# Kernel optimization log

Measured on AMD Instinct MI355X. Metric: run time of the kernel, lower is better.

Reference implementation:

```python
import jax, jax.numpy as jnp
import numpy as np

B, C, H, W = 8, 512, 32, 32
NUM_HEADS = 8
HEAD_DIM = C // NUM_HEADS


def setup_inputs() -> dict:
    key = jax.random.key(0)
    k1, k2, k3 = jax.random.split(key, 3)
    s = 0.02
    return {
        "x": jax.random.normal(k1, (B, C, H, W), dtype=jnp.float32),
        "W_qkv": jax.random.normal(k2, (3 * C, C), dtype=jnp.float32) * s,
        "b_qkv": jnp.zeros((3 * C,), dtype=jnp.float32),
        "W_proj": jax.random.normal(k3, (C, C), dtype=jnp.float32) * s,
        "b_proj": jnp.zeros((C,), dtype=jnp.float32),
    }


def reference(x, W_qkv, b_qkv, W_proj, b_proj):
    b, c, h, w = x.shape
    n = h * w  # seq_len in raster order
    nh, hd = NUM_HEADS, c // NUM_HEADS
    scale = hd ** -0.5

    # b c h w -> b n c
    x_seq = x.reshape(b, c, n).transpose(0, 2, 1)
    qkv = x_seq @ W_qkv.T + b_qkv  # (b, n, 3c)
    # b n (3 nh hd) -> 3, b, nh, n, hd
    qkv = qkv.reshape(b, n, 3, nh, hd).transpose(2, 0, 3, 1, 4)
    q, k, v = qkv[0], qkv[1], qkv[2]

    attn = jnp.einsum('bhnd,bhmd->bhnm', q, k) * scale
    causal = jnp.tril(jnp.ones((n, n), dtype=bool))
    attn = jnp.where(causal, attn, -jnp.inf)
    attn = jax.nn.softmax(attn, axis=-1)

    out = jnp.einsum('bhnm,bhmd->bhnd', attn, v)
    out = out.transpose(0, 2, 1, 3).reshape(b, n, c)  # b n c
    out = out @ W_proj.T + b_proj
    # b (h w) c -> b c h w
    return out.transpose(0, 2, 1).reshape(b, c, h, w)
```

## Files before the change

### kernel.cpp

```cpp
#include <hip/hip_runtime.h>
#include <hip/hip_bf16.h>
#include <math.h>

#define B_  8
#define C_  512
#define N_  1024
#define NH_ 8
#define HD_ 64
#define C3_ 1536

typedef __bf16 bf16x8 __attribute__((ext_vector_type(8)));
typedef float  f32x4  __attribute__((ext_vector_type(4)));
typedef __hip_bfloat16 bf16;

__device__ __forceinline__ f32x4 mfma16(const bf16x8& a, const bf16x8& b, const f32x4& c) {
    return __builtin_amdgcn_mfma_f32_16x16x32_bf16(a, b, c, 0, 0, 0);
}

__device__ __forceinline__ void ld_lds16(const bf16* g, bf16* l_uniform) {
    __builtin_amdgcn_global_load_lds(
        (const __attribute__((address_space(1))) void*)(uintptr_t)g,
        (__attribute__((address_space(3))) void*)(uintptr_t)l_uniform,
        16, 0, 0);
}


__global__ __launch_bounds__(256) void cvt_w(const float* __restrict__ Wq,
                                             const float* __restrict__ Wp,
                                             bf16* __restrict__ Wqb,
                                             bf16* __restrict__ Wpb) {
    int i = blockIdx.x * 256 + threadIdx.x;
    if (i < C3_ * C_) Wqb[i] = __float2bfloat16(Wq[i]);
    else {
        int j = i - C3_ * C_;
        if (j < C_ * C_) Wpb[j] = __float2bfloat16(Wp[j]);
    }
}

__global__ __launch_bounds__(256) void transpose_x(const float* __restrict__ x,
                                                   bf16* __restrict__ xb) {
    __shared__ float T[32][33];
    const int n0 = blockIdx.x * 32, c0 = blockIdx.y * 32, b = blockIdx.z;
    const int tx = threadIdx.x, ty = threadIdx.y;
    const float* xp = x + ((size_t)b * C_ + c0) * N_ + n0;
#pragma unroll
    for (int l = 0; l < 4; ++l)
        T[ty + 8 * l][tx] = xp[(ty + 8 * l) * N_ + tx];
    __syncthreads();
    bf16* xo = xb + ((size_t)b * N_ + n0) * C_ + c0;
#pragma unroll
    for (int l = 0; l < 4; ++l)
        xo[(ty + 8 * l) * C_ + tx] = __float2bfloat16(T[tx][ty + 8 * l]);
}

__global__ __launch_bounds__(256) void qkv_mfma(const bf16* __restrict__ xb,
                                                const bf16* __restrict__ Wqb,
                                                const float* __restrict__ bq,
                                                bf16* __restrict__ Qb,
                                                bf16* __restrict__ Kb,
                                                bf16* __restrict__ Vt) {
    __shared__ bf16 As[128 * 32];
    __shared__ bf16 Bs[128 * 32];
    __shared__ bf16 Vl[4][16][20];
    const int tid = threadIdx.x, w = tid >> 6, lane = tid & 63;
    const int lo = lane & 15, hi = lane >> 4;
    const int j0 = blockIdx.x * 128;
    const int m0 = blockIdx.y * 128;
    const int b  = m0 >> 10;

    const int srow = w * 32 + (lane >> 2);
    const int scol = (lane & 3) * 8;
    const bf16* gA = xb  + (size_t)(m0 + srow) * C_ + scol;
    const bf16* gB = Wqb + (size_t)(j0 + srow) * C_ + scol;
    bf16* lA = As + (w * 32) * 32;
    bf16* lB = Bs + (w * 32) * 32;

    f32x4 acc[4][4];
#pragma unroll
    for (int mt = 0; mt < 4; ++mt)
#pragma unroll
        for (int jt = 0; jt < 4; ++jt)
            acc[mt][jt] = (f32x4){0.f, 0.f, 0.f, 0.f};

    for (int k0 = 0; k0 < C_; k0 += 32) {
        ld_lds16(gA + k0, lA);
        ld_lds16(gA + (size_t)16 * C_ + k0, lA + 16 * 32);
        ld_lds16(gB + k0, lB);
        ld_lds16(gB + (size_t)16 * C_ + k0, lB + 16 * 32);
        __syncthreads();

        bf16x8 af[4], bfr[4];
#pragma unroll
        for (int mt = 0; mt < 4; ++mt)
            af[mt] = *(const bf16x8*)(As + ((w & 1) * 64 + mt * 16 + lo) * 32 + hi * 8);
#pragma unroll
        for (int jt = 0; jt < 4; ++jt)
            bfr[jt] = *(const bf16x8*)(Bs + ((w >> 1) * 64 + jt * 16 + lo) * 32 + hi * 8);
#pragma unroll
        for (int mt = 0; mt < 4; ++mt)
#pragma unroll
            for (int jt = 0; jt < 4; ++jt)
                acc[mt][jt] = mfma16(af[mt], bfr[jt], acc[mt][jt]);
        __syncthreads();
    }

    const int jb = (w >> 1) * 64;
    const int nbase = (m0 & 1023) + (w & 1) * 64;
#pragma unroll
    for (int jt = 0; jt < 4; ++jt) {
        const int j16 = j0 + jb + jt * 16;
        const float bias = bq[j16 + lo];
        if (j16 < 512) {
            const int h = j16 >> 6, d = (j16 & 63) + lo;
            bf16* qp = Qb + ((size_t)(b * NH_ + h) * N_) * HD_ + d;
#pragma unroll
            for (int mt = 0; mt < 4; ++mt)
#pragma unroll
                for (int r = 0; r < 4; ++r) {
                    int n = nbase + mt * 16 + hi * 4 + r;
                    qp[(size_t)n * HD_] = __float2bfloat16((acc[mt][jt][r] + bias) * 0.125f);
                }
        } else if (j16 < 1024) {
            const int jj = j16 - 512;
            const int h = jj >> 6, d = (jj & 63) + lo;
            bf16* kp = Kb + ((size_t)(b * NH_ + h) * N_) * HD_ + d;
#pragma unroll
            for (int mt = 0; mt < 4; ++mt)
#pragma unroll
                for (int r = 0; r < 4; ++r) {
                    int n = nbase + mt * 16 + hi * 4 + r;
                    kp[(size_t)n * HD_] = __float2bfloat16(acc[mt][jt][r] + bias);
                }
        } else {
            const int jj = j16 - 1024;
            const int h = jj >> 6, dbase = jj & 63;
            bf16* vp = Vt + ((size_t)(b * NH_ + h) * HD_ + dbase) * N_ + nbase;
#pragma unroll
            for (int mt = 0; mt < 4; ++mt) {
#pragma unroll
                for (int r = 0; r < 4; ++r)
                    Vl[w][hi * 4 + r][lo] = __float2bfloat16(acc[mt][jt][r] + bias);
#pragma unroll
                for (int r = 0; r < 4; ++r)
                    vp[(size_t)(hi * 4 + r) * N_ + mt * 16 + lo] = Vl[w][lo][hi * 4 + r];
            }
        }
    }
}


__global__ __launch_bounds__(256) void attn_mfma(const bf16* __restrict__ Qb,
                                                 const bf16* __restrict__ Kb,
                                                 const bf16* __restrict__ Vt,
                                                 bf16* __restrict__ ao) {
    __shared__ bf16 Ks0[64 * 32], Ks1[64 * 32];
    __shared__ bf16 Vs0[64 * 32], Vs1[64 * 32];
    __shared__ __align__(16) bf16 Pl[4][2][2][16][40];

    const int tid  = threadIdx.x;
    const int wv   = tid >> 6;
    const int lane = tid & 63;
    const int lo   = lane & 15;
    const int hi   = lane >> 4;
    const int bh   = blockIdx.x & 63;
    const int blk  = blockIdx.x >> 6;
    const int pi   = blk * 4 + wv;
    const int qwA  = pi * 16;
    const int qwB  = (63 - pi) * 16;

    const bf16* Qh = Qb + (size_t)bh * N_ * HD_;
    const bf16* Kh = Kb + (size_t)bh * N_ * HD_;
    const bf16* Vh = Vt + (size_t)bh * HD_ * N_;

    const bf16x8 qA0 = *(const bf16x8*)(Qh + (qwA + lo) * HD_ + hi * 8);
    const bf16x8 qA1 = *(const bf16x8*)(Qh + (qwA + lo) * HD_ + 32 + hi * 8);
    const bf16x8 qB0 = *(const bf16x8*)(Qh + (qwB + lo) * HD_ + hi * 8);
    const bf16x8 qB1 = *(const bf16x8*)(Qh + (qwB + lo) * HD_ + 32 + hi * 8);

    const int srow = tid >> 2;
    const int scol = (tid & 3) * 8;
    const bf16* gK = Kh + (size_t)srow * HD_ + scol;
    const bf16* gV = Vh + (size_t)srow * N_ + scol;
    bf16* lK0 = Ks0 + wv * 512;
    bf16* lK1 = Ks1 + wv * 512;
    bf16* lV0 = Vs0 + wv * 512;
    bf16* lV1 = Vs1 + wv * 512;

    f32x4 OA[4], OB[4];
    float LA[4], LB[4];
#pragma unroll
    for (int r = 0; r < 4; ++r) {
        OA[0][r] = OA[1][r] = OA[2][r] = OA[3][r] = 0.f;
        OB[0][r] = OB[1][r] = OB[2][r] = OB[3][r] = 0.f;
        LA[r] = 0.f; LB[r] = 0.f;
    }

    const int nkbA   = (qwA + 79) >> 6;
    const int nkbB   = (qwB + 79) >> 6;
    const int nkbBlk = ((63 - blk * 4) * 16 + 79) >> 6;

    for (int kb = 0; kb < nkbBlk; ++kb) {
        const int key0 = kb * 64;

        ld_lds16(gK + (size_t)key0 * HD_,      lK0);
        ld_lds16(gK + (size_t)key0 * HD_ + 32, lK1);
        ld_lds16(gV + key0,                    lV0);
        ld_lds16(gV + key0 + 32,               lV1);
        __syncthreads();

        if (kb < nkbB) {
            const bool doA = (kb < nkbA);

            bf16x8 kf[4][2], vf[4][2];
#pragma unroll
            for (int t = 0; t < 4; ++t) {
                kf[t][0] = *(const bf16x8*)(Ks0 + (t * 16 + lo) * 32 + hi * 8);
                kf[t][1] = *(const bf16x8*)(Ks1 + (t * 16 + lo) * 32 + hi * 8);
                vf[t][0] = *(const bf16x8*)(Vs0 + (t * 16 + lo) * 32 + hi * 8);
                vf[t][1] = *(const bf16x8*)(Vs1 + (t * 16 + lo) * 32 + hi * 8);
            }

            f32x4 SB[4], SA[4];
#pragma unroll
            for (int t = 0; t < 4; ++t) {
                SB[t] = (f32x4){0.f, 0.f, 0.f, 0.f};
                SB[t] = mfma16(qB0, kf[t][0], SB[t]);
                SB[t] = mfma16(qB1, kf[t][1], SB[t]);
            }
            if (doA) {
#pragma unroll
                for (int t = 0; t < 4; ++t) {
                    SA[t] = (f32x4){0.f, 0.f, 0.f, 0.f};
                    SA[t] = mfma16(qA0, kf[t][0], SA[t]);
                    SA[t] = mfma16(qA1, kf[t][1], SA[t]);
                }
            }

            if (key0 + 63 > qwB) {
#pragma unroll
                for (int t = 0; t < 4; ++t)
#pragma unroll
                    for (int r = 0; r < 4; ++r)
                        if (key0 + t * 16 + lo > qwB + hi * 4 + r) SB[t][r] = -1e30f;
            }
            if (doA && key0 + 63 > qwA) {
#pragma unroll
                for (int t = 0; t < 4; ++t)
#pragma unroll
                    for (int r = 0; r < 4; ++r)
                        if (key0 + t * 16 + lo > qwA + hi * 4 + r) SA[t][r] = -1e30f;
            }

#pragma unroll
            for (int t = 0; t < 4; ++t)
#pragma unroll
                for (int r = 0; r < 4; ++r) {
                    float p = __expf(SB[t][r]);
                    LB[r] += p;
                    Pl[wv][1][t >> 1][hi * 4 + r][(t & 1) * 16 + lo] = __float2bfloat16(p);
                }
            if (doA) {
#pragma unroll
                for (int t = 0; t < 4; ++t)
#pragma unroll
                    for (int r = 0; r < 4; ++r) {
                        float p = __expf(SA[t][r]);
                        LA[r] += p;
                        Pl[wv][0][t >> 1][hi * 4 + r][(t & 1) * 16 + lo] = __float2bfloat16(p);
                    }
            }

            bf16x8 paB0 = *(const bf16x8*)(&Pl[wv][1][0][lo][hi * 8]);
            bf16x8 paB1 = *(const bf16x8*)(&Pl[wv][1][1][lo][hi * 8]);
#pragma unroll
            for (int t = 0; t < 4; ++t) {
                OB[t] = mfma16(paB0, vf[t][0], OB[t]);
                OB[t] = mfma16(paB1, vf[t][1], OB[t]);
            }
            if (doA) {
                bf16x8 paA0 = *(const bf16x8*)(&Pl[wv][0][0][lo][hi * 8]);
                bf16x8 paA1 = *(const bf16x8*)(&Pl[wv][0][1][lo][hi * 8]);
#pragma unroll
                for (int t = 0; t < 4; ++t) {
                    OA[t] = mfma16(paA0, vf[t][0], OA[t]);
                    OA[t] = mfma16(paA1, vf[t][1], OA[t]);
                }
            }
        }
        __syncthreads();
    }

    const int b = bh >> 3, h = bh & 7;
#pragma unroll
    for (int c = 0; c < 2; ++c) {
        const int qw = c ? qwB : qwA;
        f32x4* O = c ? OB : OA;
        float* Lp = c ? LB : LA;
        float rL[4];
#pragma unroll
        for (int r = 0; r < 4; ++r) {
            float Ls = Lp[r];
#pragma unroll
            for (int off = 1; off < 16; off <<= 1)
                Ls += __shfl_xor(Ls, off, 64);
            rL[r] = 1.f / Ls;
        }
#pragma unroll
        for (int t = 0; t < 4; ++t)
#pragma unroll
            for (int r = 0; r < 4; ++r) {
                int q = qw + hi * 4 + r;
                ao[((size_t)b * N_ + q) * C_ + h * HD_ + t * 16 + lo] =
                    __float2bfloat16(O[t][r] * rL[r]);
            }
    }
}

__global__ __launch_bounds__(256) void proj_mfma(const bf16* __restrict__ aob,
                                                 const bf16* __restrict__ Wpb,
                                                 const float* __restrict__ bp,
                                                 float* __restrict__ out) {
    __shared__ bf16 As[64 * 32];
    __shared__ bf16 Bs[128 * 32];
    const int tid = threadIdx.x, w = tid >> 6, lane = tid & 63;
    const int lo = lane & 15, hi = lane >> 4;
    const int j0 = blockIdx.x * 64;
    const int n0 = blockIdx.y * 128;
    const int b  = n0 >> 10;

    const int r4 = lane >> 2, c8 = (lane & 3) * 8;
    const bf16* gA = Wpb + (size_t)(j0 + w * 16 + r4) * C_ + c8;
    const bf16* gB = aob + (size_t)(n0 + w * 32 + r4) * C_ + c8;
    bf16* lA = As + (w * 16) * 32;
    bf16* lB = Bs + (w * 32) * 32;

    f32x4 acc[2][4];
#pragma unroll
    for (int mt = 0; mt < 2; ++mt)
#pragma unroll
        for (int jt = 0; jt < 4; ++jt)
            acc[mt][jt] = (f32x4){0.f, 0.f, 0.f, 0.f};

    for (int k0 = 0; k0 < C_; k0 += 32) {
        ld_lds16(gA + k0, lA);
        ld_lds16(gB + k0, lB);
        ld_lds16(gB + (size_t)16 * C_ + k0, lB + 16 * 32);
        __syncthreads();

        bf16x8 af[2], bfr[4];
#pragma unroll
        for (int mt = 0; mt < 2; ++mt)
            af[mt] = *(const bf16x8*)(As + ((w & 1) * 32 + mt * 16 + lo) * 32 + hi * 8);
#pragma unroll
        for (int jt = 0; jt < 4; ++jt)
            bfr[jt] = *(const bf16x8*)(Bs + ((w >> 1) * 64 + jt * 16 + lo) * 32 + hi * 8);
#pragma unroll
        for (int mt = 0; mt < 2; ++mt)
#pragma unroll
            for (int jt = 0; jt < 4; ++jt)
                acc[mt][jt] = mfma16(af[mt], bfr[jt], acc[mt][jt]);
        __syncthreads();
    }

#pragma unroll
    for (int mt = 0; mt < 2; ++mt)
#pragma unroll
        for (int r = 0; r < 4; ++r) {
            const int j = j0 + (w & 1) * 32 + mt * 16 + hi * 4 + r;
            const float bias = bp[j];
            float* op = out + ((size_t)(b * C_ + j)) * N_ + (n0 & 1023) + (w >> 1) * 64 + lo;
#pragma unroll
            for (int jt = 0; jt < 4; ++jt)
                op[jt * 16] = acc[mt][jt][r] + bias;
        }
}

extern "C" void kernel_launch(void* const* d_in, const int* in_sizes, int n_in,
                              void* d_out, int out_size, void* d_ws, size_t ws_size,
                              hipStream_t stream) {
    const float* x  = (const float*)d_in[0];
    const float* Wq = (const float*)d_in[1];
    const float* bq = (const float*)d_in[2];
    const float* Wp = (const float*)d_in[3];
    const float* bp = (const float*)d_in[4];
    float* out = (float*)d_out;

    const size_t headElems = (size_t)B_ * NH_ * N_ * HD_;
    bf16* xb  = (bf16*)d_ws;
    bf16* Wqb = xb + (size_t)B_ * N_ * C_;
    bf16* Wpb = Wqb + (size_t)C3_ * C_;
    bf16* Qb  = Wpb + (size_t)C_ * C_;
    bf16* Kb  = Qb + headElems;
    bf16* Vt  = Kb + headElems;
    bf16* aob = Vt + headElems;

    cvt_w<<<dim3((C3_ * C_ + C_ * C_ + 255) / 256), dim3(256), 0, stream>>>(Wq, Wp, Wqb, Wpb);
    transpose_x<<<dim3(N_ / 32, C_ / 32, B_), dim3(32, 8), 0, stream>>>(x, xb);

    qkv_mfma<<<dim3(C3_ / 128, (B_ * N_) / 128), dim3(256), 0, stream>>>(xb, Wqb, bq, Qb, Kb, Vt);
    attn_mfma<<<dim3(8 * 64), dim3(256), 0, stream>>>(Qb, Kb, Vt, aob);
    proj_mfma<<<dim3(C_ / 64, (B_ * N_) / 128), dim3(256), 0, stream>>>(aob, Wpb, bp, out);
}
```

Measured before the change: 142.4 us.

## Double-buffer attention K/V tiles and fuse input prep kernels

```diff
diff --git a/kernel.cpp b/kernel.cpp
--- a/kernel.cpp
+++ b/kernel.cpp
@@ -9,8 +9,9 @@
 #define HD_ 64
 #define C3_ 1536
 
-typedef __bf16 bf16x8 __attribute__((ext_vector_type(8)));
-typedef float  f32x4  __attribute__((ext_vector_type(4)));
+typedef __bf16 bf16x8  __attribute__((ext_vector_type(8)));
+typedef __bf16 bf16x4v __attribute__((ext_vector_type(4)));
+typedef float  f32x4   __attribute__((ext_vector_type(4)));
 typedef __hip_bfloat16 bf16;
 
 __device__ __forceinline__ f32x4 mfma16(const bf16x8& a, const bf16x8& b, const f32x4& c) {
@@ -24,33 +25,42 @@
         16, 0, 0);
 }
 
-
-__global__ __launch_bounds__(256) void cvt_w(const float* __restrict__ Wq,
-                                             const float* __restrict__ Wp,
-                                             bf16* __restrict__ Wqb,
-                                             bf16* __restrict__ Wpb) {
-    int i = blockIdx.x * 256 + threadIdx.x;
-    if (i < C3_ * C_) Wqb[i] = __float2bfloat16(Wq[i]);
-    else {
-        int j = i - C3_ * C_;
-        if (j < C_ * C_) Wpb[j] = __float2bfloat16(Wp[j]);
-    }
-}
-
-__global__ __launch_bounds__(256) void transpose_x(const float* __restrict__ x,
-                                                   bf16* __restrict__ xb) {
-    __shared__ float T[32][33];
-    const int n0 = blockIdx.x * 32, c0 = blockIdx.y * 32, b = blockIdx.z;
-    const int tx = threadIdx.x, ty = threadIdx.y;
-    const float* xp = x + ((size_t)b * C_ + c0) * N_ + n0;
-#pragma unroll
-    for (int l = 0; l < 4; ++l)
-        T[ty + 8 * l][tx] = xp[(ty + 8 * l) * N_ + tx];
-    __syncthreads();
-    bf16* xo = xb + ((size_t)b * N_ + n0) * C_ + c0;
-#pragma unroll
-    for (int l = 0; l < 4; ++l)
-        xo[(ty + 8 * l) * C_ + tx] = __float2bfloat16(T[tx][ty + 8 * l]);
+__global__ __launch_bounds__(256) void prep(const float* __restrict__ x,
+                                            const float* __restrict__ Wq,
+                                            const float* __restrict__ Wp,
+                                            bf16* __restrict__ xb,
+                                            bf16* __restrict__ Wqb,
+                                            bf16* __restrict__ Wpb) {
+    const int tid = threadIdx.x;
+    if (blockIdx.x < 4096) {
+        __shared__ float T[32][33];
+        int t = blockIdx.x;
+        const int n0 = (t & 31) * 32; t >>= 5;
+        const int c0 = (t & 15) * 32; t >>= 4;
+        const int b  = t;
+        const int tx = tid & 31, ty = tid >> 5;
+        const float* xp = x + ((size_t)b * C_ + c0) * N_ + n0;
+#pragma unroll
+        for (int l = 0; l < 4; ++l)
+            T[ty + 8 * l][tx] = xp[(ty + 8 * l) * N_ + tx];
+        __syncthreads();
+        bf16* xo = xb + ((size_t)b * N_ + n0) * C_ + c0;
+#pragma unroll
+        for (int l = 0; l < 4; ++l)
+            xo[(ty + 8 * l) * C_ + tx] = __float2bfloat16(T[tx][ty + 8 * l]);
+    } else {
+        const int base = (blockIdx.x - 4096) * 1024 + tid * 4;
+        const float* src;
+        bf16* dst;
+        int off;
+        if (base < C3_ * C_) { src = Wq; dst = Wqb; off = base; }
+        else                 { src = Wp; dst = Wpb; off = base - C3_ * C_; }
+        f32x4 w = *(const f32x4*)(src + off);
+        bf16x4v o;
+#pragma unroll
+        for (int i = 0; i < 4; ++i) o[i] = (__bf16)w[i];
+        *(bf16x4v*)(dst + off) = o;
+    }
 }
 
 __global__ __launch_bounds__(256) void qkv_mfma(const bf16* __restrict__ xb,
@@ -153,8 +163,8 @@
                                                  const bf16* __restrict__ Kb,
                                                  const bf16* __restrict__ Vt,
                                                  bf16* __restrict__ ao) {
-    __shared__ bf16 Ks0[64 * 32], Ks1[64 * 32];
-    __shared__ bf16 Vs0[64 * 32], Vs1[64 * 32];
+    __shared__ bf16 Ks0[2][64 * 32], Ks1[2][64 * 32];
+    __shared__ bf16 Vs0[2][64 * 32], Vs1[2][64 * 32];
     __shared__ __align__(16) bf16 Pl[4][2][2][16][40];
 
     const int tid  = threadIdx.x;
@@ -181,10 +191,7 @@
     const int scol = (tid & 3) * 8;
     const bf16* gK = Kh + (size_t)srow * HD_ + scol;
     const bf16* gV = Vh + (size_t)srow * N_ + scol;
-    bf16* lK0 = Ks0 + wv * 512;
-    bf16* lK1 = Ks1 + wv * 512;
-    bf16* lV0 = Vs0 + wv * 512;
-    bf16* lV1 = Vs1 + wv * 512;
+    const int lofs = wv * 512;
 
     f32x4 OA[4], OB[4];
     float LA[4], LB[4];
@@ -199,14 +206,26 @@
     const int nkbB   = (qwB + 79) >> 6;
     const int nkbBlk = ((63 - blk * 4) * 16 + 79) >> 6;
 
+    {
+        ld_lds16(gK,      Ks0[0] + lofs);
+        ld_lds16(gK + 32, Ks1[0] + lofs);
+        ld_lds16(gV,      Vs0[0] + lofs);
+        ld_lds16(gV + 32, Vs1[0] + lofs);
+    }
+
     for (int kb = 0; kb < nkbBlk; ++kb) {
         const int key0 = kb * 64;
-
-        ld_lds16(gK + (size_t)key0 * HD_,      lK0);
-        ld_lds16(gK + (size_t)key0 * HD_ + 32, lK1);
-        ld_lds16(gV + key0,                    lV0);
-        ld_lds16(gV + key0 + 32,               lV1);
-        __syncthreads();
+        const int cur  = kb & 1;
+
+        __syncthreads();
+
+        if (kb + 1 < nkbBlk) {
+            const size_t nk = (size_t)(key0 + 64);
+            ld_lds16(gK + nk * HD_,      Ks0[cur ^ 1] + lofs);
+            ld_lds16(gK + nk * HD_ + 32, Ks1[cur ^ 1] + lofs);
+            ld_lds16(gV + nk,            Vs0[cur ^ 1] + lofs);
+            ld_lds16(gV + nk + 32,       Vs1[cur ^ 1] + lofs);
+        }
 
         if (kb < nkbB) {
             const bool doA = (kb < nkbA);
@@ -214,10 +233,10 @@
             bf16x8 kf[4][2], vf[4][2];
 #pragma unroll
             for (int t = 0; t < 4; ++t) {
-                kf[t][0] = *(const bf16x8*)(Ks0 + (t * 16 + lo) * 32 + hi * 8);
-                kf[t][1] = *(const bf16x8*)(Ks1 + (t * 16 + lo) * 32 + hi * 8);
-                vf[t][0] = *(const bf16x8*)(Vs0 + (t * 16 + lo) * 32 + hi * 8);
-                vf[t][1] = *(const bf16x8*)(Vs1 + (t * 16 + lo) * 32 + hi * 8);
+                kf[t][0] = *(const bf16x8*)(Ks0[cur] + (t * 16 + lo) * 32 + hi * 8);
+                kf[t][1] = *(const bf16x8*)(Ks1[cur] + (t * 16 + lo) * 32 + hi * 8);
+                vf[t][0] = *(const bf16x8*)(Vs0[cur] + (t * 16 + lo) * 32 + hi * 8);
+                vf[t][1] = *(const bf16x8*)(Vs1[cur] + (t * 16 + lo) * 32 + hi * 8);
             }
 
             f32x4 SB[4], SA[4];
@@ -287,7 +306,6 @@
                 }
             }
         }
-        __syncthreads();
     }
 
     const int b = bh >> 3, h = bh & 7;
@@ -394,8 +412,7 @@
     bf16* Vt  = Kb + headElems;
     bf16* aob = Vt + headElems;
 
-    cvt_w<<<dim3((C3_ * C_ + C_ * C_ + 255) / 256), dim3(256), 0, stream>>>(Wq, Wp, Wqb, Wpb);
-    transpose_x<<<dim3(N_ / 32, C_ / 32, B_), dim3(32, 8), 0, stream>>>(x, xb);
+    prep<<<dim3(4096 + 1024), dim3(256), 0, stream>>>(x, Wq, Wp, xb, Wqb, Wpb);
 
     qkv_mfma<<<dim3(C3_ / 128, (B_ * N_) / 128), dim3(256), 0, stream>>>(xb, Wqb, bq, Qb, Kb, Vt);
     attn_mfma<<<dim3(8 * 64), dim3(256), 0, stream>>>(Qb, Kb, Vt, aob);
```

Result: faster. 139.4 us (-2.2%).
